# Optimization experiments

Hardware: AMD Instinct MI355X
Metric: run time of the kernel (lower is better)

## Reference

```python
import jax, jax.numpy as jnp
import numpy as np

N_USERS = 100000
N_ITEMS = 50000
NNZ = 1600000
DIM = 128


def setup_inputs() -> dict:
    key = jax.random.key(0)
    ks = jax.random.split(key, 6)
    user_emb = jax.random.normal(ks[0], (N_USERS, DIM), dtype=jnp.float32)
    item_emb = jax.random.normal(ks[1], (N_ITEMS, DIM), dtype=jnp.float32)
    hg_rows = jax.random.randint(ks[2], (NNZ,), 0, N_USERS, dtype=jnp.int32)
    hg_cols = jax.random.randint(ks[3], (NNZ,), 0, N_ITEMS, dtype=jnp.int32)
    hg_vals = jax.random.uniform(ks[4], (NNZ,), dtype=jnp.float32)
    # aggregation: nn.Linear(2*dim, dim) -> weight [dim, 2*dim], bias [dim]
    bound = 1.0 / np.sqrt(2 * DIM)
    W_agg = jax.random.uniform(ks[5], (DIM, 2 * DIM), minval=-bound, maxval=bound, dtype=jnp.float32)
    b_agg = jnp.zeros((DIM,), dtype=jnp.float32)
    return {"user_emb": user_emb, "item_emb": item_emb, "hg_rows": hg_rows,
            "hg_cols": hg_cols, "hg_vals": hg_vals, "W_agg": W_agg, "b_agg": b_agg}


def reference(user_emb, item_emb, hg_rows, hg_cols, hg_vals, W_agg, b_agg):
    n_users = user_emb.shape[0]
    n_items = item_emb.shape[0]
    # node_msg = H @ item_emb  (SpMM via gather + segment_sum)  [n_users, dim]
    gathered = hg_vals[:, None] * item_emb[hg_cols]          # [nnz, dim]
    node_msg = jax.ops.segment_sum(gathered, hg_rows, num_segments=n_users)
    # elementwise gate with user embedding
    edge_node_element = node_msg * user_emb                   # [n_users, dim]
    # msg = Linear(concat([node_msg, gated]))
    cat = jnp.concatenate([node_msg, edge_node_element], axis=1)  # [n_users, 2*dim]
    msg = cat @ W_agg.T + b_agg                               # [n_users, dim]
    # norm_emb = H.T @ msg  (transpose SpMM scatter-back)     [n_items, dim]
    scattered = hg_vals[:, None] * msg[hg_rows]               # [nnz, dim]
    norm_emb = jax.ops.segment_sum(scattered, hg_cols, num_segments=n_items)
    return (norm_emb, msg)
```

## Files before the change

kernel.cpp:

```cpp
#include <hip/hip_runtime.h>

#define DIM 128
#define NB 512

typedef short v8s __attribute__((ext_vector_type(8)));
typedef float v4f __attribute__((ext_vector_type(4)));

__device__ __forceinline__ unsigned short f2bf(float f) {
    unsigned int x = __float_as_uint(f);
    unsigned int r = ((x >> 16) & 1u) + 0x7fffu;
    return (unsigned short)((x + r) >> 16);
}
__device__ __forceinline__ float bf2f(short s) {
    return __uint_as_float(((unsigned)(unsigned short)s) << 16);
}


__global__ __launch_bounds__(256) void k_binA(const int* __restrict__ rows, const int* __restrict__ cols,
                                              int* __restrict__ Mu, int* __restrict__ Mi,
                                              int nnz, int chunk, int nbu, int nbi, int shu, int shi)
{
    __shared__ int hu[256], hi[256];
    int k = blockIdx.x, t = threadIdx.x;
    for (int j = t; j < nbu; j += 256) hu[j] = 0;
    for (int j = t; j < nbi; j += 256) hi[j] = 0;
    __syncthreads();
    int beg = k * chunk, end = min(beg + chunk, nnz);
    if (beg < end) {
        int beg4 = beg >> 2, end4 = end >> 2;
        for (int e4 = beg4 + t; e4 < end4; e4 += 256) {
            int4 r = reinterpret_cast<const int4*>(rows)[e4];
            int4 c = reinterpret_cast<const int4*>(cols)[e4];
            atomicAdd(&hu[r.x >> shu], 1); atomicAdd(&hu[r.y >> shu], 1);
            atomicAdd(&hu[r.z >> shu], 1); atomicAdd(&hu[r.w >> shu], 1);
            atomicAdd(&hi[c.x >> shi], 1); atomicAdd(&hi[c.y >> shi], 1);
            atomicAdd(&hi[c.z >> shi], 1); atomicAdd(&hi[c.w >> shi], 1);
        }
        for (int e = (end4 << 2) + t; e < end; e += 256) {
            atomicAdd(&hu[rows[e] >> shu], 1);
            atomicAdd(&hi[cols[e] >> shi], 1);
        }
    }
    __syncthreads();
    for (int j = t; j < nbu; j += 256) Mu[k * nbu + j] = hu[j];
    for (int j = t; j < nbi; j += 256) Mi[k * nbi + j] = hi[j];
}

__global__ __launch_bounds__(256) void k_binS1(int* __restrict__ M, int* __restrict__ tot,
                                               int nb, int nblk)
{
    __shared__ int ps[256];
    int j = blockIdx.x, t = threadIdx.x;
    int i0 = 2 * t, i1 = 2 * t + 1;
    int v0 = (i0 < nblk) ? M[i0 * nb + j] : 0;
    int v1 = (i1 < nblk) ? M[i1 * nb + j] : 0;
    ps[t] = v0 + v1;
    __syncthreads();
    for (int off = 1; off < 256; off <<= 1) {
        int x = (t >= off) ? ps[t - off] : 0;
        __syncthreads();
        ps[t] += x;
        __syncthreads();
    }
    int ep = ps[t] - (v0 + v1);
    if (i0 < nblk) M[i0 * nb + j] = ep;
    if (i1 < nblk) M[i1 * nb + j] = ep + v0;
    if (t == 255) tot[j] = ps[255];
}

__global__ __launch_bounds__(256) void k_binS2(const int* __restrict__ tot, int* __restrict__ base, int nb)
{
    __shared__ int s[256];
    int t = threadIdx.x;
    int v = (t < nb) ? tot[t] : 0;
    s[t] = v;
    __syncthreads();
    for (int off = 1; off < 256; off <<= 1) {
        int x = (t >= off) ? s[t - off] : 0;
        __syncthreads();
        s[t] += x;
        __syncthreads();
    }
    if (t < nb) base[t] = s[t] - v;
    if (t == 255) base[nb] = s[255];
}

__global__ __launch_bounds__(256) void k_binB(const int* __restrict__ rows, const int* __restrict__ cols,
                                              const float* __restrict__ vals,
                                              const int* __restrict__ Mu, const int* __restrict__ Mi,
                                              const int* __restrict__ base_u, const int* __restrict__ base_i,
                                              int2* __restrict__ bu, int2* __restrict__ bi,
                                              int nnz, int chunk, int nbu, int nbi, int shu, int shi)
{
    __shared__ int cu[256], ci[256];
    int k = blockIdx.x, t = threadIdx.x;
    for (int j = t; j < nbu; j += 256) cu[j] = Mu[k * nbu + j] + base_u[j];
    for (int j = t; j < nbi; j += 256) ci[j] = Mi[k * nbi + j] + base_i[j];
    __syncthreads();
    int mu = (1 << shu) - 1, mi = (1 << shi) - 1;
    int beg = k * chunk, end = min(beg + chunk, nnz);
    if (beg >= end) return;
    int beg4 = beg >> 2, end4 = end >> 2;
    for (int e4 = beg4 + t; e4 < end4; e4 += 256) {
        int4 r = reinterpret_cast<const int4*>(rows)[e4];
        int4 c = reinterpret_cast<const int4*>(cols)[e4];
        int4 v = reinterpret_cast<const int4*>(vals)[e4];
        int p;
        p = atomicAdd(&cu[r.x >> shu], 1); bu[p] = make_int2((c.x << shu) | (r.x & mu), v.x);
        p = atomicAdd(&ci[c.x >> shi], 1); bi[p] = make_int2((r.x << shi) | (c.x & mi), v.x);
        p = atomicAdd(&cu[r.y >> shu], 1); bu[p] = make_int2((c.y << shu) | (r.y & mu), v.y);
        p = atomicAdd(&ci[c.y >> shi], 1); bi[p] = make_int2((r.y << shi) | (c.y & mi), v.y);
        p = atomicAdd(&cu[r.z >> shu], 1); bu[p] = make_int2((c.z << shu) | (r.z & mu), v.z);
        p = atomicAdd(&ci[c.z >> shi], 1); bi[p] = make_int2((r.z << shi) | (c.z & mi), v.z);
        p = atomicAdd(&cu[r.w >> shu], 1); bu[p] = make_int2((c.w << shu) | (r.w & mu), v.w);
        p = atomicAdd(&ci[c.w >> shi], 1); bi[p] = make_int2((r.w << shi) | (c.w & mi), v.w);
    }
    for (int e = (end4 << 2) + t; e < end; e += 256) {
        int r = rows[e], c = cols[e];
        int v = reinterpret_cast<const int*>(vals)[e];
        int p;
        p = atomicAdd(&cu[r >> shu], 1); bu[p] = make_int2((c << shu) | (r & mu), v);
        p = atomicAdd(&ci[c >> shi], 1); bi[p] = make_int2((r << shi) | (c & mi), v);
    }
}

__global__ __launch_bounds__(256) void k_binC(const int2* __restrict__ binned,
                                              const int* __restrict__ base,
                                              int* __restrict__ ptr, int2* __restrict__ cs,
                                              int nrows, int sh, int total)
{
    __shared__ int hist[512];
    __shared__ int scn[512];
    __shared__ int psum[256];
    int j = blockIdx.x, t = threadIdx.x;
    int BR = 1 << sh;
    int row0 = j << sh;
    int beg = base[j], end = base[j + 1];
    for (int r = t; r < BR; r += 256) hist[r] = 0;
    __syncthreads();
    for (int e = beg + t; e < end; e += 256)
        atomicAdd(&hist[binned[e].x & (BR - 1)], 1);
    __syncthreads();
    int v0 = (2 * t < BR) ? hist[2 * t] : 0;
    int v1 = (2 * t + 1 < BR) ? hist[2 * t + 1] : 0;
    psum[t] = v0 + v1;
    __syncthreads();
    for (int off = 1; off < 256; off <<= 1) {
        int x = (t >= off) ? psum[t - off] : 0;
        __syncthreads();
        psum[t] += x;
        __syncthreads();
    }
    int ep = psum[t] - (v0 + v1);
    if (2 * t < BR) scn[2 * t] = ep;
    if (2 * t + 1 < BR) scn[2 * t + 1] = ep + v0;
    __syncthreads();
    for (int r = t; r < BR; r += 256) {
        int row = row0 + r;
        if (row < nrows) ptr[row] = beg + scn[r];
        hist[r] = 0;
    }
    if (j == 0 && t == 0) ptr[nrows] = total;
    __syncthreads();
    for (int e = beg + t; e < end; e += 256) {
        int2 rec = binned[e];
        int rl = rec.x & (BR - 1);
        int pos = beg + scn[rl] + atomicAdd(&hist[rl], 1);
        cs[pos] = make_int2(((unsigned)rec.x) >> sh, rec.y);
    }
}

__global__ void k_tobf(const float* __restrict__ in, unsigned short* __restrict__ out, int n8)
{
    int i = blockIdx.x * 256 + threadIdx.x;
    if (i >= n8) return;
    float4 a = reinterpret_cast<const float4*>(in)[2 * i];
    float4 c = reinterpret_cast<const float4*>(in)[2 * i + 1];
    uint4 o;
    o.x = (unsigned)f2bf(a.x) | ((unsigned)f2bf(a.y) << 16);
    o.y = (unsigned)f2bf(a.z) | ((unsigned)f2bf(a.w) << 16);
    o.z = (unsigned)f2bf(c.x) | ((unsigned)f2bf(c.y) << 16);
    o.w = (unsigned)f2bf(c.z) | ((unsigned)f2bf(c.w) << 16);
    reinterpret_cast<uint4*>(out)[i] = o;
}

__global__ __launch_bounds__(256) void k_spmm_bf(const int* __restrict__ ptr, const int2* __restrict__ pairs,
                                                 const unsigned short* __restrict__ src,
                                                 float* __restrict__ dst, int nrows)
{
    int r = blockIdx.x * 16 + (threadIdx.x >> 4);
    if (r >= nrows) return;
    int l = threadIdx.x & 15;
    int beg = ptr[r], end = ptr[r + 1];
    float a0[8], a1[8];
    #pragma unroll
    for (int k = 0; k < 8; ++k) { a0[k] = 0.f; a1[k] = 0.f; }
    int j = beg;
    for (; j + 1 < end; j += 2) {
        int2 p0 = pairs[j], p1 = pairs[j + 1];
        float v0 = __int_as_float(p0.y), v1 = __int_as_float(p1.y);
        v8s s0 = *reinterpret_cast<const v8s*>(src + (long long)p0.x * DIM + 8 * l);
        v8s s1 = *reinterpret_cast<const v8s*>(src + (long long)p1.x * DIM + 8 * l);
        #pragma unroll
        for (int k = 0; k < 8; ++k) {
            a0[k] += v0 * bf2f(s0[k]);
            a1[k] += v1 * bf2f(s1[k]);
        }
    }
    if (j < end) {
        int2 p0 = pairs[j];
        float v0 = __int_as_float(p0.y);
        v8s s0 = *reinterpret_cast<const v8s*>(src + (long long)p0.x * DIM + 8 * l);
        #pragma unroll
        for (int k = 0; k < 8; ++k) a0[k] += v0 * bf2f(s0[k]);
    }
    float4 o0, o1;
    o0.x = a0[0] + a1[0]; o0.y = a0[1] + a1[1]; o0.z = a0[2] + a1[2]; o0.w = a0[3] + a1[3];
    o1.x = a0[4] + a1[4]; o1.y = a0[5] + a1[5]; o1.z = a0[6] + a1[6]; o1.w = a0[7] + a1[7];
    float* dp = dst + (long long)r * DIM + 8 * l;
    *reinterpret_cast<float4*>(dp) = o0;
    *reinterpret_cast<float4*>(dp + 4) = o1;
}

__global__ __launch_bounds__(256) void k_spmm4(const int* __restrict__ ptr, const int2* __restrict__ pairs,
                                               const float* __restrict__ src, float* __restrict__ dst, int nrows)
{
    int r = blockIdx.x * 8 + (threadIdx.x >> 5);
    if (r >= nrows) return;
    int l = threadIdx.x & 31;
    int beg = ptr[r], end = ptr[r + 1];
    float4 a0 = {0.f, 0.f, 0.f, 0.f}, a1 = {0.f, 0.f, 0.f, 0.f};
    int j = beg;
    for (; j + 1 < end; j += 2) {
        int2 p0 = pairs[j], p1 = pairs[j + 1];
        float v0 = __int_as_float(p0.y), v1 = __int_as_float(p1.y);
        float4 s0 = *reinterpret_cast<const float4*>(src + (long long)p0.x * DIM + 4 * l);
        float4 s1 = *reinterpret_cast<const float4*>(src + (long long)p1.x * DIM + 4 * l);
        a0.x += v0 * s0.x; a0.y += v0 * s0.y; a0.z += v0 * s0.z; a0.w += v0 * s0.w;
        a1.x += v1 * s1.x; a1.y += v1 * s1.y; a1.z += v1 * s1.z; a1.w += v1 * s1.w;
    }
    if (j < end) {
        int2 p0 = pairs[j];
        float v0 = __int_as_float(p0.y);
        float4 s0 = *reinterpret_cast<const float4*>(src + (long long)p0.x * DIM + 4 * l);
        a0.x += v0 * s0.x; a0.y += v0 * s0.y; a0.z += v0 * s0.z; a0.w += v0 * s0.w;
    }
    a0.x += a1.x; a0.y += a1.y; a0.z += a1.z; a0.w += a1.w;
    *reinterpret_cast<float4*>(dst + (long long)r * DIM + 4 * l) = a0;
}

__global__ void k_bsw(const float* __restrict__ W, unsigned short* __restrict__ Bsw)
{
    int i = blockIdx.x * 256 + threadIdx.x;
    int kt = i >> 12;
    int rem = i & 4095;
    int c = rem >> 5;
    int kk = rem & 31;
    Bsw[i] = f2bf(W[c * 256 + kt * 32 + kk]);
}

__global__ __launch_bounds__(256) void k_msg5(const float* __restrict__ nm_in,
                                              const float* __restrict__ ue,
                                              const unsigned short* __restrict__ Bsw,
                                              const float* __restrict__ b,
                                              float* __restrict__ msg,
                                              unsigned short* __restrict__ msg_bf, int nu)
{
    __shared__ unsigned short cat[64 * 264];
    int tid = threadIdx.x;
    int u0 = blockIdx.x * 64;

    for (int idx = tid; idx < 2048; idx += 256) {
        int u = idx >> 5, d4 = idx & 31;
        float4 nm4 = make_float4(0.f, 0.f, 0.f, 0.f);
        float4 ue4 = make_float4(0.f, 0.f, 0.f, 0.f);
        if (u0 + u < nu) {
            long long p = (long long)(u0 + u) * DIM + d4 * 4;
            nm4 = *reinterpret_cast<const float4*>(nm_in + p);
            ue4 = *reinterpret_cast<const float4*>(ue + p);
        }
        unsigned short* row = cat + u * 264;
        uint2 nmp, gp;
        nmp.x = (unsigned)f2bf(nm4.x) | ((unsigned)f2bf(nm4.y) << 16);
        nmp.y = (unsigned)f2bf(nm4.z) | ((unsigned)f2bf(nm4.w) << 16);
        gp.x  = (unsigned)f2bf(nm4.x * ue4.x) | ((unsigned)f2bf(nm4.y * ue4.y) << 16);
        gp.y  = (unsigned)f2bf(nm4.z * ue4.z) | ((unsigned)f2bf(nm4.w * ue4.w) << 16);
        *reinterpret_cast<uint2*>(row + d4 * 4) = nmp;
        *reinterpret_cast<uint2*>(row + 128 + d4 * 4) = gp;
    }
    __syncthreads();

    int l = tid & 63, w = tid >> 6;
    int lr = l & 15, hi = l >> 4;
    v4f acc[8];
    #pragma unroll
    for (int ct = 0; ct < 8; ++ct) acc[ct] = (v4f){0.f, 0.f, 0.f, 0.f};

    const unsigned short* arow = cat + (w * 16 + lr) * 264;
    for (int kt = 0; kt < 8; ++kt) {
        v8s a = *reinterpret_cast<const v8s*>(arow + kt * 32 + hi * 8);
        #pragma unroll
        for (int ct = 0; ct < 8; ++ct) {
            v8s bb = *reinterpret_cast<const v8s*>(Bsw + kt * 4096 + (ct * 16 + lr) * 32 + hi * 8);
            acc[ct] = __builtin_amdgcn_mfma_f32_16x16x32_bf16(a, bb, acc[ct], 0, 0, 0);
        }
    }

    int ub = u0 + w * 16 + hi * 4;
    #pragma unroll
    for (int ct = 0; ct < 8; ++ct) {
        float bc = b[ct * 16 + lr];
        #pragma unroll
        for (int j = 0; j < 4; ++j) {
            int u = ub + j;
            if (u < nu) {
                float val = acc[ct][j] + bc;
                long long p = (long long)u * DIM + ct * 16 + lr;
                msg[p] = val;
                msg_bf[p] = f2bf(val);
            }
        }
    }
}

__global__ void k_wt(const float* __restrict__ W, float* __restrict__ Wt)
{
    int t = blockIdx.x * 256 + threadIdx.x;
    int k = t >> 7;
    int c = t & 127;
    Wt[t] = W[c * 256 + k];
}

#define UPB 32
#define CATP 260

__global__ __launch_bounds__(256) void k_msg4(const float* __restrict__ nm_in,
                                              const float* __restrict__ ue,
                                              const float* __restrict__ Wt,
                                              const float* __restrict__ b,
                                              float* __restrict__ msg, int nu)
{
    __shared__ float cat[UPB * CATP];
    int tid = threadIdx.x;
    int u0 = blockIdx.x * UPB;
    for (int idx = tid; idx < UPB * DIM; idx += 256) {
        int u = idx >> 7, d = idx & 127;
        float nm = 0.f, g = 0.f;
        if (u0 + u < nu) {
            long long p = (long long)(u0 + u) * DIM + d;
            nm = nm_in[p];
            g = nm * ue[p];
        }
        cat[u * CATP + d] = nm;
        cat[u * CATP + DIM + d] = g;
    }
    __syncthreads();

    int tc = tid & 31;
    int tu = tid >> 5;
    float acc[4][4];
    #pragma unroll
    for (int r = 0; r < 4; ++r)
        #pragma unroll
        for (int c = 0; c < 4; ++c) acc[r][c] = 0.f;

    const float* cbase = &cat[(tu * 4) * CATP];
    for (int k4 = 0; k4 < 64; ++k4) {
        float4 w[4];
        #pragma unroll
        for (int kk = 0; kk < 4; ++kk)
            w[kk] = *reinterpret_cast<const float4*>(Wt + (k4 * 4 + kk) * DIM + tc * 4);
        #pragma unroll
        for (int r = 0; r < 4; ++r) {
            float4 a = *reinterpret_cast<const float4*>(cbase + r * CATP + k4 * 4);
            acc[r][0] += a.x * w[0].x + a.y * w[1].x + a.z * w[2].x + a.w * w[3].x;
            acc[r][1] += a.x * w[0].y + a.y * w[1].y + a.z * w[2].y + a.w * w[3].y;
            acc[r][2] += a.x * w[0].z + a.y * w[1].z + a.z * w[2].z + a.w * w[3].z;
            acc[r][3] += a.x * w[0].w + a.y * w[1].w + a.z * w[2].w + a.w * w[3].w;
        }
    }

    float4 bb = *reinterpret_cast<const float4*>(b + tc * 4);
    #pragma unroll
    for (int r = 0; r < 4; ++r) {
        int u = u0 + tu * 4 + r;
        if (u < nu) {
            float4 o;
            o.x = acc[r][0] + bb.x; o.y = acc[r][1] + bb.y;
            o.z = acc[r][2] + bb.z; o.w = acc[r][3] + bb.w;
            *reinterpret_cast<float4*>(msg + (long long)u * DIM + tc * 4) = o;
        }
    }
}


__global__ void k_count(const int* __restrict__ rows, const int* __restrict__ cols,
                        int* __restrict__ cnt_u, int* __restrict__ cnt_i, int nnz4, int nnz)
{
    int i = blockIdx.x * blockDim.x + threadIdx.x;
    int stride = gridDim.x * blockDim.x;
    for (int e4 = i; e4 < nnz4; e4 += stride) {
        int4 r = reinterpret_cast<const int4*>(rows)[e4];
        int4 c = reinterpret_cast<const int4*>(cols)[e4];
        atomicAdd(&cnt_u[r.x], 1); atomicAdd(&cnt_u[r.y], 1);
        atomicAdd(&cnt_u[r.z], 1); atomicAdd(&cnt_u[r.w], 1);
        atomicAdd(&cnt_i[c.x], 1); atomicAdd(&cnt_i[c.y], 1);
        atomicAdd(&cnt_i[c.z], 1); atomicAdd(&cnt_i[c.w], 1);
    }
    for (int e = nnz4 * 4 + i; e < nnz; e += stride) {
        atomicAdd(&cnt_u[rows[e]], 1);
        atomicAdd(&cnt_i[cols[e]], 1);
    }
}

__global__ void k_scan1(const int* __restrict__ cnt, int* __restrict__ ptr,
                        int* __restrict__ partial, int n)
{
    __shared__ int s[256];
    int i = blockIdx.x * 256 + threadIdx.x;
    int v = (i < n) ? cnt[i] : 0;
    s[threadIdx.x] = v;
    __syncthreads();
    for (int off = 1; off < 256; off <<= 1) {
        int x = (threadIdx.x >= off) ? s[threadIdx.x - off] : 0;
        __syncthreads();
        s[threadIdx.x] += x;
        __syncthreads();
    }
    if (i < n) ptr[i] = s[threadIdx.x] - v;
    if (threadIdx.x == 255) partial[blockIdx.x] = s[255];
}

__global__ void k_scan2(int* __restrict__ partial, int n)
{
    __shared__ int s[512];
    int v = (threadIdx.x < (unsigned)n) ? partial[threadIdx.x] : 0;
    s[threadIdx.x] = v;
    __syncthreads();
    for (int off = 1; off < 512; off <<= 1) {
        int x = (threadIdx.x >= off) ? s[threadIdx.x - off] : 0;
        __syncthreads();
        s[threadIdx.x] += x;
        __syncthreads();
    }
    if (threadIdx.x < (unsigned)n) partial[threadIdx.x] = s[threadIdx.x] - v;
}

__global__ void k_scan3(int* __restrict__ ptr, const int* __restrict__ partial,
                        int* __restrict__ woff, int n, int total)
{
    int i = blockIdx.x * 256 + threadIdx.x;
    if (i < n) {
        int p = ptr[i] + partial[blockIdx.x];
        ptr[i] = p;
        woff[i] = p;
        if (i == n - 1) ptr[n] = total;
    }
}

__global__ void k_edge_scatter(const int* __restrict__ rows, const int* __restrict__ cols,
                               const float* __restrict__ vals,
                               int* __restrict__ woff_u, int* __restrict__ woff_i,
                               int2* __restrict__ cs_u, int2* __restrict__ cs_i,
                               int nnz4, int nnz)
{
    int i = blockIdx.x * blockDim.x + threadIdx.x;
    int stride = gridDim.x * blockDim.x;
    for (int e4 = i; e4 < nnz4; e4 += stride) {
        int4 r = reinterpret_cast<const int4*>(rows)[e4];
        int4 c = reinterpret_cast<const int4*>(cols)[e4];
        float4 v = reinterpret_cast<const float4*>(vals)[e4];
        int pu, pi;
        pu = atomicAdd(&woff_u[r.x], 1); cs_u[pu] = make_int2(c.x, __float_as_int(v.x));
        pi = atomicAdd(&woff_i[c.x], 1); cs_i[pi] = make_int2(r.x, __float_as_int(v.x));
        pu = atomicAdd(&woff_u[r.y], 1); cs_u[pu] = make_int2(c.y, __float_as_int(v.y));
        pi = atomicAdd(&woff_i[c.y], 1); cs_i[pi] = make_int2(r.y, __float_as_int(v.y));
        pu = atomicAdd(&woff_u[r.z], 1); cs_u[pu] = make_int2(c.z, __float_as_int(v.z));
        pi = atomicAdd(&woff_i[c.z], 1); cs_i[pi] = make_int2(r.z, __float_as_int(v.z));
        pu = atomicAdd(&woff_u[r.w], 1); cs_u[pu] = make_int2(c.w, __float_as_int(v.w));
        pi = atomicAdd(&woff_i[c.w], 1); cs_i[pi] = make_int2(r.w, __float_as_int(v.w));
    }
    for (int e = nnz4 * 4 + i; e < nnz; e += stride) {
        int r = rows[e], c = cols[e];
        float v = vals[e];
        int pu = atomicAdd(&woff_u[r], 1); cs_u[pu] = make_int2(c, __float_as_int(v));
        int pi = atomicAdd(&woff_i[c], 1); cs_i[pi] = make_int2(r, __float_as_int(v));
    }
}


__global__ void k_scatter(const int* __restrict__ didx, const int* __restrict__ sidx,
                          const float* __restrict__ vals, const float* __restrict__ src,
                          float* __restrict__ dst, long long nnz)
{
    long long t = (long long)blockIdx.x * blockDim.x + threadIdx.x;
    long long total = nnz * 32;
    if (t >= total) return;
    long long e = t >> 5;
    int d = (int)(t & 31) * 4;
    int si = sidx[e];
    int di = didx[e];
    float v = vals[e];
    const float4 s = *reinterpret_cast<const float4*>(src + (long long)si * DIM + d);
    float* p = dst + (long long)di * DIM + d;
    atomicAdd(p + 0, v * s.x);
    atomicAdd(p + 1, v * s.y);
    atomicAdd(p + 2, v * s.z);
    atomicAdd(p + 3, v * s.w);
}

__global__ void k_msg_simple(const float* __restrict__ user_emb, const float* __restrict__ W,
                             const float* __restrict__ b, float* __restrict__ msg)
{
    __shared__ float cat[2 * DIM];
    int u = blockIdx.x;
    int t = threadIdx.x;
    long long base = (long long)u * DIM;
    float nm = msg[base + t];
    float ue = user_emb[base + t];
    cat[t] = nm;
    cat[DIM + t] = nm * ue;
    __syncthreads();
    float acc = b[t];
    const float4* Wr = reinterpret_cast<const float4*>(W + (long long)t * 2 * DIM);
    const float4* c4 = reinterpret_cast<const float4*>(cat);
    #pragma unroll
    for (int k = 0; k < 2 * DIM / 4; ++k) {
        float4 w = Wr[k];
        float4 c = c4[k];
        acc += w.x * c.x + w.y * c.y + w.z * c.z + w.w * c.w;
    }
    msg[base + t] = acc;
}


extern "C" void kernel_launch(void* const* d_in, const int* in_sizes, int n_in,
                              void* d_out, int out_size, void* d_ws, size_t ws_size,
                              hipStream_t stream) {
    const float* user_emb = (const float*)d_in[0];
    const float* item_emb = (const float*)d_in[1];
    const int*   rows     = (const int*)d_in[2];
    const int*   cols     = (const int*)d_in[3];
    const float* vals     = (const float*)d_in[4];
    const float* W        = (const float*)d_in[5];
    const float* b        = (const float*)d_in[6];

    int nu = in_sizes[0] / DIM;
    int ni = in_sizes[1] / DIM;
    int nnz = in_sizes[2];

    float* norm_emb = (float*)d_out;
    float* msg      = (float*)d_out + (long long)ni * DIM;

    auto align256 = [](size_t x) { return (x + 255) & ~(size_t)255; };

    int shu = 0; while ((((long long)nu + (1LL << shu) - 1) >> shu) > 256) shu++;
    int shi = 0; while ((((long long)ni + (1LL << shi) - 1) >> shi) > 256) shi++;
    int nbu = (int)(((long long)nu + (1LL << shu) - 1) >> shu);
    int nbi = (int)(((long long)ni + (1LL << shi) - 1) >> shi);
    int chunk = (((nnz + NB - 1) / NB) + 3) & ~3;

    size_t off = 0;
    size_t o_bu    = off; off = align256(off + (size_t)nnz * 8);
    size_t o_bi    = off; off = align256(off + (size_t)nnz * 8);
    size_t o_csu   = off; off = align256(off + (size_t)nnz * 8);
    size_t o_Mu    = off; off = align256(off + (size_t)NB * nbu * 4);
    size_t o_Mi    = off; off = align256(off + (size_t)NB * nbi * 4);
    size_t o_totu  = off; off = align256(off + (size_t)nbu * 4);
    size_t o_toti  = off; off = align256(off + (size_t)nbi * 4);
    size_t o_baseu = off; off = align256(off + (size_t)(nbu + 1) * 4);
    size_t o_basei = off; off = align256(off + (size_t)(nbi + 1) * 4);
    size_t o_ptru  = off; off = align256(off + (size_t)(nu + 1) * 4);
    size_t o_ptri  = off; off = align256(off + (size_t)(ni + 1) * 4);
    size_t o_bsw   = off; off = align256(off + (size_t)32768 * 2);
    size_t need_binned = off;

    size_t itbf_need  = (size_t)ni * DIM * 2;
    size_t msgbf_need = (size_t)nu * DIM * 2;
    size_t o_itbf, o_msgbf;
    bool alias_it  = (o_csu - o_bi) >= itbf_need;
    bool alias_msg = (o_Mu - o_bi) >= msgbf_need;
    if (alias_it) o_itbf = o_bi;
    else { o_itbf = need_binned; need_binned = align256(need_binned + itbf_need); }
    if (alias_msg) o_msgbf = o_bi;
    else { o_msgbf = need_binned; need_binned = align256(need_binned + msgbf_need); }

    bool pack_ok = ((long long)ni < (1LL << (31 - shu))) && ((long long)nu < (1LL << (31 - shi)))
                   && (shu <= 9) && (shi <= 9);

    off = 0;
    size_t o_cs_u   = off; off = align256(off + (size_t)nnz * 8);
    size_t o_cs_i   = off; off = align256(off + (size_t)nnz * 8);
    size_t o_ptr_u  = off; off = align256(off + (size_t)(nu + 1) * 4);
    size_t o_ptr_i  = off; off = align256(off + (size_t)(ni + 1) * 4);
    size_t o_woff_u = off; off = align256(off + (size_t)nu * 4);
    size_t o_woff_i = off; off = align256(off + (size_t)ni * 4);
    size_t o_part_u = off; off = align256(off + 512 * 4);
    size_t o_part_i = off; off = align256(off + 512 * 4);
    size_t o_wt2    = off; off = align256(off + (size_t)256 * DIM * 4);
    size_t need_r5 = off;

    int npb_u = (nu + 255) / 256;
    int npb_i = (ni + 255) / 256;

    char* ws = (char*)d_ws;

    if (ws_size >= need_binned && pack_ok) {
        int2* bu     = (int2*)(ws + o_bu);
        int2* bi     = (int2*)(ws + o_bi);
        int2* cs_u   = (int2*)(ws + o_csu);
        int2* cs_i   = (int2*)(ws + o_bu);
        int*  Mu     = (int*)(ws + o_Mu);
        int*  Mi     = (int*)(ws + o_Mi);
        int*  totu   = (int*)(ws + o_totu);
        int*  toti   = (int*)(ws + o_toti);
        int*  baseu  = (int*)(ws + o_baseu);
        int*  basei  = (int*)(ws + o_basei);
        int*  ptr_u  = (int*)(ws + o_ptru);
        int*  ptr_i  = (int*)(ws + o_ptri);
        unsigned short* bsw   = (unsigned short*)(ws + o_bsw);
        unsigned short* itbf  = (unsigned short*)(ws + o_itbf);
        unsigned short* msgbf = (unsigned short*)(ws + o_msgbf);

        k_binA<<<NB, 256, 0, stream>>>(rows, cols, Mu, Mi, nnz, chunk, nbu, nbi, shu, shi);
        k_bsw<<<128, 256, 0, stream>>>(W, bsw);
        k_binS1<<<nbu, 256, 0, stream>>>(Mu, totu, nbu, NB);
        k_binS1<<<nbi, 256, 0, stream>>>(Mi, toti, nbi, NB);
        k_binS2<<<1, 256, 0, stream>>>(totu, baseu, nbu);
        k_binS2<<<1, 256, 0, stream>>>(toti, basei, nbi);
        k_binB<<<NB, 256, 0, stream>>>(rows, cols, vals, Mu, Mi, baseu, basei,
                                       bu, bi, nnz, chunk, nbu, nbi, shu, shi);
        k_binC<<<nbu, 256, 0, stream>>>(bu, baseu, ptr_u, cs_u, nu, shu, nnz);
        k_binC<<<nbi, 256, 0, stream>>>(bi, basei, ptr_i, cs_i, ni, shi, nnz);

        int n8i = ni * DIM / 8;
        k_tobf<<<(n8i + 255) / 256, 256, 0, stream>>>(item_emb, itbf, n8i);

        k_spmm_bf<<<(nu + 15) / 16, 256, 0, stream>>>(ptr_u, cs_u, itbf, msg, nu);
        k_msg5<<<(nu + 63) / 64, 256, 0, stream>>>(msg, user_emb, bsw, b, msg, msgbf, nu);
        k_spmm_bf<<<(ni + 15) / 16, 256, 0, stream>>>(ptr_i, cs_i, msgbf, norm_emb, ni);
    } else if (ws_size >= need_r5 && npb_u <= 512 && npb_i <= 512) {
        int2*  cs_u   = (int2*)(ws + o_cs_u);
        int2*  cs_i   = (int2*)(ws + o_cs_i);
        int*   ptr_u  = (int*)(ws + o_ptr_u);
        int*   ptr_i  = (int*)(ws + o_ptr_i);
        int*   woff_u = (int*)(ws + o_woff_u);
        int*   woff_i = (int*)(ws + o_woff_i);
        int*   part_u = (int*)(ws + o_part_u);
        int*   part_i = (int*)(ws + o_part_i);
        float* wt     = (float*)(ws + o_wt2);

        hipMemsetAsync(woff_u, 0, (size_t)nu * 4, stream);
        hipMemsetAsync(woff_i, 0, (size_t)ni * 4, stream);

        int nnz4 = nnz / 4;
        int gs = 1024;
        k_count<<<gs, 256, 0, stream>>>(rows, cols, woff_u, woff_i, nnz4, nnz);
        k_wt<<<(256 * DIM) / 256, 256, 0, stream>>>(W, wt);

        k_scan1<<<npb_u, 256, 0, stream>>>(woff_u, ptr_u, part_u, nu);
        k_scan1<<<npb_i, 256, 0, stream>>>(woff_i, ptr_i, part_i, ni);
        k_scan2<<<1, 512, 0, stream>>>(part_u, npb_u);
        k_scan2<<<1, 512, 0, stream>>>(part_i, npb_i);
        k_scan3<<<npb_u, 256, 0, stream>>>(ptr_u, part_u, woff_u, nu, nnz);
        k_scan3<<<npb_i, 256, 0, stream>>>(ptr_i, part_i, woff_i, ni, nnz);

        k_edge_scatter<<<gs, 256, 0, stream>>>(rows, cols, vals, woff_u, woff_i,
                                               cs_u, cs_i, nnz4, nnz);

        k_spmm4<<<(nu + 7) / 8, 256, 0, stream>>>(ptr_u, cs_u, item_emb, msg, nu);
        k_msg4<<<(nu + UPB - 1) / UPB, 256, 0, stream>>>(msg, user_emb, wt, b, msg, nu);
        k_spmm4<<<(ni + 7) / 8, 256, 0, stream>>>(ptr_i, cs_i, msg, norm_emb, ni);
    } else {
        hipMemsetAsync(d_out, 0, (size_t)out_size * sizeof(float), stream);
        long long tot = (long long)nnz * 32;
        int blk = 256;
        long long nblk = (tot + blk - 1) / blk;
        k_scatter<<<(int)nblk, blk, 0, stream>>>(rows, cols, vals, item_emb, msg, nnz);
        k_msg_simple<<<nu, DIM, 0, stream>>>(user_emb, W, b, msg);
        k_scatter<<<(int)nblk, blk, 0, stream>>>(cols, rows, vals, msg, norm_emb, nnz);
    }
}
```

Baseline: 278.6 us.

## Fuse user-side SpMM with gating and MFMA linear layer into one kernel

Adds a single-wavefront kernel that gathers bf16 item rows per user, applies the user-embedding gate, stages the concatenated bf16 row in shared memory and runs the 256x128 linear layer with MFMA, writing msg and its bf16 copy. This removes the fp32 node_msg write and re-read between the SpMM and linear kernels, plus one launch. The msg bf16 buffer gets its own workspace region so it no longer aliases the binning buffer still in use. The cost is 64-thread blocks, each thread walking four users serially, and a fallback to the old path when workspace is too small.

```diff
diff --git a/kernel.cpp b/kernel.cpp
--- a/kernel.cpp
+++ b/kernel.cpp
@@ -259,6 +259,101 @@
     Bsw[i] = f2bf(W[c * 256 + kt * 32 + kk]);
 }
 
+__global__ __launch_bounds__(64) void k_fused64(const int* __restrict__ ptr,
+                                                const int2* __restrict__ pairs,
+                                                const unsigned short* __restrict__ itbf,
+                                                const float* __restrict__ ue,
+                                                const unsigned short* __restrict__ Bsw,
+                                                const float* __restrict__ b,
+                                                float* __restrict__ msg,
+                                                unsigned short* __restrict__ msg_bf, int nu)
+{
+    __shared__ unsigned short cat[16 * 264];
+    int l = threadIdx.x;
+    int u0 = blockIdx.x * 16;
+    int lr = l & 15, hi = l >> 4;
+    int d = lr * 8;
+
+    #pragma unroll
+    for (int p = 0; p < 4; ++p) {
+        int ur = p * 4 + hi;
+        int u = u0 + ur;
+        float a0[8], a1[8];
+        #pragma unroll
+        for (int k = 0; k < 8; ++k) { a0[k] = 0.f; a1[k] = 0.f; }
+        float4 ue0 = make_float4(0.f,0.f,0.f,0.f), ue1 = make_float4(0.f,0.f,0.f,0.f);
+        if (u < nu) {
+            int beg = ptr[u], end = ptr[u + 1];
+            int j = beg;
+            for (; j + 1 < end; j += 2) {
+                int2 p0 = pairs[j], p1 = pairs[j + 1];
+                float v0 = __int_as_float(p0.y), v1 = __int_as_float(p1.y);
+                v8s s0 = *reinterpret_cast<const v8s*>(itbf + (long long)p0.x * DIM + d);
+                v8s s1 = *reinterpret_cast<const v8s*>(itbf + (long long)p1.x * DIM + d);
+                #pragma unroll
+                for (int k = 0; k < 8; ++k) {
+                    a0[k] += v0 * bf2f(s0[k]);
+                    a1[k] += v1 * bf2f(s1[k]);
+                }
+            }
+            if (j < end) {
+                int2 p0 = pairs[j];
+                float v0 = __int_as_float(p0.y);
+                v8s s0 = *reinterpret_cast<const v8s*>(itbf + (long long)p0.x * DIM + d);
+                #pragma unroll
+                for (int k = 0; k < 8; ++k) a0[k] += v0 * bf2f(s0[k]);
+            }
+            ue0 = *reinterpret_cast<const float4*>(ue + (long long)u * DIM + d);
+            ue1 = *reinterpret_cast<const float4*>(ue + (long long)u * DIM + d + 4);
+        }
+        float nm[8];
+        #pragma unroll
+        for (int k = 0; k < 8; ++k) nm[k] = a0[k] + a1[k];
+        float uev[8] = {ue0.x, ue0.y, ue0.z, ue0.w, ue1.x, ue1.y, ue1.z, ue1.w};
+        uint4 nmp, gp;
+        nmp.x = (unsigned)f2bf(nm[0]) | ((unsigned)f2bf(nm[1]) << 16);
+        nmp.y = (unsigned)f2bf(nm[2]) | ((unsigned)f2bf(nm[3]) << 16);
+        nmp.z = (unsigned)f2bf(nm[4]) | ((unsigned)f2bf(nm[5]) << 16);
+        nmp.w = (unsigned)f2bf(nm[6]) | ((unsigned)f2bf(nm[7]) << 16);
+        gp.x = (unsigned)f2bf(nm[0] * uev[0]) | ((unsigned)f2bf(nm[1] * uev[1]) << 16);
+        gp.y = (unsigned)f2bf(nm[2] * uev[2]) | ((unsigned)f2bf(nm[3] * uev[3]) << 16);
+        gp.z = (unsigned)f2bf(nm[4] * uev[4]) | ((unsigned)f2bf(nm[5] * uev[5]) << 16);
+        gp.w = (unsigned)f2bf(nm[6] * uev[6]) | ((unsigned)f2bf(nm[7] * uev[7]) << 16);
+        *reinterpret_cast<uint4*>(cat + ur * 264 + d) = nmp;
+        *reinterpret_cast<uint4*>(cat + ur * 264 + 128 + d) = gp;
+    }
+    __syncthreads();
+
+    v4f acc[8];
+    #pragma unroll
+    for (int ct = 0; ct < 8; ++ct) acc[ct] = (v4f){0.f, 0.f, 0.f, 0.f};
+    const unsigned short* arow = cat + lr * 264;
+    for (int kt = 0; kt < 8; ++kt) {
+        v8s a = *reinterpret_cast<const v8s*>(arow + kt * 32 + hi * 8);
+        #pragma unroll
+        for (int ct = 0; ct < 8; ++ct) {
+            v8s bb = *reinterpret_cast<const v8s*>(Bsw + kt * 4096 + (ct * 16 + lr) * 32 + hi * 8);
+            acc[ct] = __builtin_amdgcn_mfma_f32_16x16x32_bf16(a, bb, acc[ct], 0, 0, 0);
+        }
+    }
+
+    int ub = u0 + hi * 4;
+    #pragma unroll
+    for (int ct = 0; ct < 8; ++ct) {
+        float bc = b[ct * 16 + lr];
+        #pragma unroll
+        for (int j = 0; j < 4; ++j) {
+            int u = ub + j;
+            if (u < nu) {
+                float val = acc[ct][j] + bc;
+                long long p = (long long)u * DIM + ct * 16 + lr;
+                msg[p] = val;
+                msg_bf[p] = f2bf(val);
+            }
+        }
+    }
+}
+
 __global__ __launch_bounds__(256) void k_msg5(const float* __restrict__ nm_in,
                                               const float* __restrict__ ue,
                                               const unsigned short* __restrict__ Bsw,
@@ -573,17 +668,25 @@
     size_t o_ptru  = off; off = align256(off + (size_t)(nu + 1) * 4);
     size_t o_ptri  = off; off = align256(off + (size_t)(ni + 1) * 4);
     size_t o_bsw   = off; off = align256(off + (size_t)32768 * 2);
-    size_t need_binned = off;
+    size_t need_base = off;
 
     size_t itbf_need  = (size_t)ni * DIM * 2;
     size_t msgbf_need = (size_t)nu * DIM * 2;
-    size_t o_itbf, o_msgbf;
-    bool alias_it  = (o_csu - o_bi) >= itbf_need;
+    bool alias_it = (o_csu - o_bi) >= itbf_need;
+
+    size_t need_fused = need_base;
+    size_t o_msgbf_f = need_fused; need_fused = align256(need_fused + msgbf_need);
+    size_t o_itbf_f;
+    if (alias_it) o_itbf_f = o_bi;
+    else { o_itbf_f = need_fused; need_fused = align256(need_fused + itbf_need); }
+
+    size_t need_r9 = need_base;
     bool alias_msg = (o_Mu - o_bi) >= msgbf_need;
-    if (alias_it) o_itbf = o_bi;
-    else { o_itbf = need_binned; need_binned = align256(need_binned + itbf_need); }
-    if (alias_msg) o_msgbf = o_bi;
-    else { o_msgbf = need_binned; need_binned = align256(need_binned + msgbf_need); }
+    size_t o_itbf_9, o_msgbf_9;
+    if (alias_it) o_itbf_9 = o_bi;
+    else { o_itbf_9 = need_r9; need_r9 = align256(need_r9 + itbf_need); }
+    if (alias_msg) o_msgbf_9 = o_bi;
+    else { o_msgbf_9 = need_r9; need_r9 = align256(need_r9 + msgbf_need); }
 
     bool pack_ok = ((long long)ni < (1LL << (31 - shu))) && ((long long)nu < (1LL << (31 - shi)))
                    && (shu <= 9) && (shi <= 9);
@@ -605,7 +708,8 @@
 
     char* ws = (char*)d_ws;
 
-    if (ws_size >= need_binned && pack_ok) {
+    if (pack_ok && (ws_size >= need_fused || ws_size >= need_r9)) {
+        bool fused = (ws_size >= need_fused);
         int2* bu     = (int2*)(ws + o_bu);
         int2* bi     = (int2*)(ws + o_bi);
         int2* cs_u   = (int2*)(ws + o_csu);
@@ -619,8 +723,8 @@
         int*  ptr_u  = (int*)(ws + o_ptru);
         int*  ptr_i  = (int*)(ws + o_ptri);
         unsigned short* bsw   = (unsigned short*)(ws + o_bsw);
-        unsigned short* itbf  = (unsigned short*)(ws + o_itbf);
-        unsigned short* msgbf = (unsigned short*)(ws + o_msgbf);
+        unsigned short* itbf  = (unsigned short*)(ws + (fused ? o_itbf_f : o_itbf_9));
+        unsigned short* msgbf = (unsigned short*)(ws + (fused ? o_msgbf_f : o_msgbf_9));
 
         k_binA<<<NB, 256, 0, stream>>>(rows, cols, Mu, Mi, nnz, chunk, nbu, nbi, shu, shi);
         k_bsw<<<128, 256, 0, stream>>>(W, bsw);
@@ -636,8 +740,13 @@
         int n8i = ni * DIM / 8;
         k_tobf<<<(n8i + 255) / 256, 256, 0, stream>>>(item_emb, itbf, n8i);
 
-        k_spmm_bf<<<(nu + 15) / 16, 256, 0, stream>>>(ptr_u, cs_u, itbf, msg, nu);
-        k_msg5<<<(nu + 63) / 64, 256, 0, stream>>>(msg, user_emb, bsw, b, msg, msgbf, nu);
+        if (fused) {
+            k_fused64<<<(nu + 15) / 16, 64, 0, stream>>>(ptr_u, cs_u, itbf, user_emb,
+                                                         bsw, b, msg, msgbf, nu);
+        } else {
+            k_spmm_bf<<<(nu + 15) / 16, 256, 0, stream>>>(ptr_u, cs_u, itbf, msg, nu);
+            k_msg5<<<(nu + 63) / 64, 256, 0, stream>>>(msg, user_emb, bsw, b, msg, msgbf, nu);
+        }
         k_spmm_bf<<<(ni + 15) / 16, 256, 0, stream>>>(ptr_i, cs_i, msgbf, norm_emb, ni);
     } else if (ws_size >= need_r5 && npb_u <= 512 && npb_i <= 512) {
         int2*  cs_u   = (int2*)(ws + o_cs_u);
```

Result: no change. 275.4 us (-1.2%).

## Fuse user SpMM gather into MFMA linear kernel and merge binning launches

Applied to the files above, without the earlier changes.

Fuses the user-side SpMM gather with the gate and the bf16 MFMA linear layer, so node_msg no longer makes an fp32 round trip through global memory. The binning scan and compaction kernels for users and items are merged into single launches to cut launch count. The SpMM gather is rewritten so each 16-lane group handles two rows, with pair indices loaded cooperatively and broadcast by shuffles, giving 16 outstanding loads per iteration. The workspace now gives cs_i and msgbf their own regions instead of aliasing, which raises the memory footprint.

```diff
diff --git a/kernel.cpp b/kernel.cpp
--- a/kernel.cpp
+++ b/kernel.cpp
@@ -46,14 +46,18 @@
     for (int j = t; j < nbi; j += 256) Mi[k * nbi + j] = hi[j];
 }
 
-__global__ __launch_bounds__(256) void k_binS1(int* __restrict__ M, int* __restrict__ tot,
-                                               int nb, int nblk)
+__global__ __launch_bounds__(256) void k_binS1m(int* __restrict__ Mu, int* __restrict__ totu, int nbu,
+                                                int* __restrict__ Mi, int* __restrict__ toti, int nbi,
+                                                int nblk)
 {
     __shared__ int ps[256];
     int j = blockIdx.x, t = threadIdx.x;
+    int* M; int* tot; int nb; int col;
+    if (j < nbu) { M = Mu; tot = totu; nb = nbu; col = j; }
+    else         { M = Mi; tot = toti; nb = nbi; col = j - nbu; }
     int i0 = 2 * t, i1 = 2 * t + 1;
-    int v0 = (i0 < nblk) ? M[i0 * nb + j] : 0;
-    int v1 = (i1 < nblk) ? M[i1 * nb + j] : 0;
+    int v0 = (i0 < nblk) ? M[i0 * nb + col] : 0;
+    int v1 = (i1 < nblk) ? M[i1 * nb + col] : 0;
     ps[t] = v0 + v1;
     __syncthreads();
     for (int off = 1; off < 256; off <<= 1) {
@@ -63,15 +67,19 @@
         __syncthreads();
     }
     int ep = ps[t] - (v0 + v1);
-    if (i0 < nblk) M[i0 * nb + j] = ep;
-    if (i1 < nblk) M[i1 * nb + j] = ep + v0;
-    if (t == 255) tot[j] = ps[255];
-}
-
-__global__ __launch_bounds__(256) void k_binS2(const int* __restrict__ tot, int* __restrict__ base, int nb)
+    if (i0 < nblk) M[i0 * nb + col] = ep;
+    if (i1 < nblk) M[i1 * nb + col] = ep + v0;
+    if (t == 255) tot[col] = ps[255];
+}
+
+__global__ __launch_bounds__(256) void k_binS2m(const int* __restrict__ totu, int* __restrict__ baseu, int nbu,
+                                                const int* __restrict__ toti, int* __restrict__ basei, int nbi)
 {
     __shared__ int s[256];
     int t = threadIdx.x;
+    const int* tot; int* base; int nb;
+    if (blockIdx.x == 0) { tot = totu; base = baseu; nb = nbu; }
+    else                 { tot = toti; base = basei; nb = nbi; }
     int v = (t < nb) ? tot[t] : 0;
     s[t] = v;
     __syncthreads();
@@ -124,18 +132,22 @@
     }
 }
 
-__global__ __launch_bounds__(256) void k_binC(const int2* __restrict__ binned,
-                                              const int* __restrict__ base,
-                                              int* __restrict__ ptr, int2* __restrict__ cs,
-                                              int nrows, int sh, int total)
+__global__ __launch_bounds__(256) void k_binCm(const int2* __restrict__ bu, const int* __restrict__ baseu,
+                                               int* __restrict__ ptru, int2* __restrict__ csu, int nu_, int shu,
+                                               const int2* __restrict__ bi, const int* __restrict__ basei,
+                                               int* __restrict__ ptri, int2* __restrict__ csi, int ni_, int shi,
+                                               int nbu, int total)
 {
     __shared__ int hist[512];
     __shared__ int scn[512];
     __shared__ int psum[256];
     int j = blockIdx.x, t = threadIdx.x;
+    const int2* binned; const int* base; int* ptr; int2* cs; int nrows, sh, lj;
+    if (j < nbu) { binned = bu; base = baseu; ptr = ptru; cs = csu; nrows = nu_; sh = shu; lj = j; }
+    else         { binned = bi; base = basei; ptr = ptri; cs = csi; nrows = ni_; sh = shi; lj = j - nbu; }
     int BR = 1 << sh;
-    int row0 = j << sh;
-    int beg = base[j], end = base[j + 1];
+    int row0 = lj << sh;
+    int beg = base[lj], end = base[lj + 1];
     for (int r = t; r < BR; r += 256) hist[r] = 0;
     __syncthreads();
     for (int e = beg + t; e < end; e += 256)
@@ -160,7 +172,7 @@
         if (row < nrows) ptr[row] = beg + scn[r];
         hist[r] = 0;
     }
-    if (j == 0 && t == 0) ptr[nrows] = total;
+    if (lj == 0 && t == 0) ptr[nrows] = total;
     __syncthreads();
     for (int e = beg + t; e < end; e += 256) {
         int2 rec = binned[e];
@@ -184,42 +196,81 @@
     reinterpret_cast<uint4*>(out)[i] = o;
 }
 
+__device__ __forceinline__ void gather8x2(const int2* __restrict__ pairs,
+                                          const unsigned short* __restrict__ src,
+                                          int b0, int e0, int b1, int e1,
+                                          int lr, int gb,
+                                          float* __restrict__ acc0,
+                                          float* __restrict__ acc1)
+{
+    while (b0 < e0 || b1 < e1) {
+        int2 pl = make_int2(0, 0);
+        if (lr < 8) {
+            if (b0 + lr < e0) pl = pairs[b0 + lr];
+        } else {
+            int o = lr - 8;
+            if (b1 + o < e1) pl = pairs[b1 + o];
+        }
+        int   idx[16];
+        float vv[16];
+        #pragma unroll
+        for (int e = 0; e < 16; ++e) {
+            idx[e] = __shfl(pl.x, gb + e, 64);
+            vv[e]  = __int_as_float(__shfl(pl.y, gb + e, 64));
+        }
+        v8s sa[8], sb[8];
+        #pragma unroll
+        for (int e = 0; e < 8; ++e)
+            sa[e] = *reinterpret_cast<const v8s*>(src + (long long)idx[e] * DIM + 8 * lr);
+        #pragma unroll
+        for (int e = 0; e < 8; ++e)
+            sb[e] = *reinterpret_cast<const v8s*>(src + (long long)idx[8 + e] * DIM + 8 * lr);
+        #pragma unroll
+        for (int e = 0; e < 8; ++e) {
+            #pragma unroll
+            for (int k = 0; k < 8; ++k)
+                acc0[k] += vv[e] * bf2f(sa[e][k]);
+        }
+        #pragma unroll
+        for (int e = 0; e < 8; ++e) {
+            #pragma unroll
+            for (int k = 0; k < 8; ++k)
+                acc1[k] += vv[8 + e] * bf2f(sb[e][k]);
+        }
+        b0 += 8; b1 += 8;
+    }
+}
+
 __global__ __launch_bounds__(256) void k_spmm_bf(const int* __restrict__ ptr, const int2* __restrict__ pairs,
                                                  const unsigned short* __restrict__ src,
                                                  float* __restrict__ dst, int nrows)
 {
-    int r = blockIdx.x * 16 + (threadIdx.x >> 4);
-    if (r >= nrows) return;
-    int l = threadIdx.x & 15;
-    int beg = ptr[r], end = ptr[r + 1];
-    float a0[8], a1[8];
+    int g = threadIdx.x >> 4;
+    int r0 = blockIdx.x * 32 + g;
+    int r1 = r0 + 16;
+    int lr = threadIdx.x & 15;
+    int gb = (threadIdx.x & 63) & ~15;
+    int b0 = 0, e0 = 0, b1 = 0, e1 = 0;
+    if (r0 < nrows) { b0 = ptr[r0]; e0 = ptr[r0 + 1]; }
+    if (r1 < nrows) { b1 = ptr[r1]; e1 = ptr[r1 + 1]; }
+    float acc0[8], acc1[8];
     #pragma unroll
-    for (int k = 0; k < 8; ++k) { a0[k] = 0.f; a1[k] = 0.f; }
-    int j = beg;
-    for (; j + 1 < end; j += 2) {
-        int2 p0 = pairs[j], p1 = pairs[j + 1];
-        float v0 = __int_as_float(p0.y), v1 = __int_as_float(p1.y);
-        v8s s0 = *reinterpret_cast<const v8s*>(src + (long long)p0.x * DIM + 8 * l);
-        v8s s1 = *reinterpret_cast<const v8s*>(src + (long long)p1.x * DIM + 8 * l);
-        #pragma unroll
-        for (int k = 0; k < 8; ++k) {
-            a0[k] += v0 * bf2f(s0[k]);
-            a1[k] += v1 * bf2f(s1[k]);
-        }
-    }
-    if (j < end) {
-        int2 p0 = pairs[j];
-        float v0 = __int_as_float(p0.y);
-        v8s s0 = *reinterpret_cast<const v8s*>(src + (long long)p0.x * DIM + 8 * l);
-        #pragma unroll
-        for (int k = 0; k < 8; ++k) a0[k] += v0 * bf2f(s0[k]);
-    }
-    float4 o0, o1;
-    o0.x = a0[0] + a1[0]; o0.y = a0[1] + a1[1]; o0.z = a0[2] + a1[2]; o0.w = a0[3] + a1[3];
-    o1.x = a0[4] + a1[4]; o1.y = a0[5] + a1[5]; o1.z = a0[6] + a1[6]; o1.w = a0[7] + a1[7];
-    float* dp = dst + (long long)r * DIM + 8 * l;
-    *reinterpret_cast<float4*>(dp) = o0;
-    *reinterpret_cast<float4*>(dp + 4) = o1;
+    for (int k = 0; k < 8; ++k) { acc0[k] = 0.f; acc1[k] = 0.f; }
+    gather8x2(pairs, src, b0, e0, b1, e1, lr, gb, acc0, acc1);
+    if (r0 < nrows) {
+        float* dp = dst + (long long)r0 * DIM + 8 * lr;
+        float4 o0 = {acc0[0], acc0[1], acc0[2], acc0[3]};
+        float4 o1 = {acc0[4], acc0[5], acc0[6], acc0[7]};
+        *reinterpret_cast<float4*>(dp) = o0;
+        *reinterpret_cast<float4*>(dp + 4) = o1;
+    }
+    if (r1 < nrows) {
+        float* dp = dst + (long long)r1 * DIM + 8 * lr;
+        float4 o0 = {acc1[0], acc1[1], acc1[2], acc1[3]};
+        float4 o1 = {acc1[4], acc1[5], acc1[6], acc1[7]};
+        *reinterpret_cast<float4*>(dp) = o0;
+        *reinterpret_cast<float4*>(dp + 4) = o1;
+    }
 }
 
 __global__ __launch_bounds__(256) void k_spmm4(const int* __restrict__ ptr, const int2* __restrict__ pairs,
@@ -259,62 +310,99 @@
     Bsw[i] = f2bf(W[c * 256 + kt * 32 + kk]);
 }
 
-__global__ __launch_bounds__(256) void k_msg5(const float* __restrict__ nm_in,
-                                              const float* __restrict__ ue,
-                                              const unsigned short* __restrict__ Bsw,
-                                              const float* __restrict__ b,
-                                              float* __restrict__ msg,
-                                              unsigned short* __restrict__ msg_bf, int nu)
-{
-    __shared__ unsigned short cat[64 * 264];
+__global__ __launch_bounds__(256) void k_fused(const int* __restrict__ ptr,
+                                               const int2* __restrict__ pairs,
+                                               const unsigned short* __restrict__ itbf,
+                                               const float* __restrict__ ue,
+                                               const unsigned short* __restrict__ Bsw,
+                                               const float* __restrict__ b,
+                                               float* __restrict__ msg,
+                                               unsigned short* __restrict__ msg_bf, int nu)
+{
+    __shared__ unsigned short cat[4][16 * 264];
     int tid = threadIdx.x;
-    int u0 = blockIdx.x * 64;
-
-    for (int idx = tid; idx < 2048; idx += 256) {
-        int u = idx >> 5, d4 = idx & 31;
-        float4 nm4 = make_float4(0.f, 0.f, 0.f, 0.f);
-        float4 ue4 = make_float4(0.f, 0.f, 0.f, 0.f);
-        if (u0 + u < nu) {
-            long long p = (long long)(u0 + u) * DIM + d4 * 4;
-            nm4 = *reinterpret_cast<const float4*>(nm_in + p);
-            ue4 = *reinterpret_cast<const float4*>(ue + p);
-        }
-        unsigned short* row = cat + u * 264;
-        uint2 nmp, gp;
-        nmp.x = (unsigned)f2bf(nm4.x) | ((unsigned)f2bf(nm4.y) << 16);
-        nmp.y = (unsigned)f2bf(nm4.z) | ((unsigned)f2bf(nm4.w) << 16);
-        gp.x  = (unsigned)f2bf(nm4.x * ue4.x) | ((unsigned)f2bf(nm4.y * ue4.y) << 16);
-        gp.y  = (unsigned)f2bf(nm4.z * ue4.z) | ((unsigned)f2bf(nm4.w * ue4.w) << 16);
-        *reinterpret_cast<uint2*>(row + d4 * 4) = nmp;
-        *reinterpret_cast<uint2*>(row + 128 + d4 * 4) = gp;
-    }
-    __syncthreads();
-
-    int l = tid & 63, w = tid >> 6;
+    int w = tid >> 6, l = tid & 63;
     int lr = l & 15, hi = l >> 4;
-    v4f acc[8];
+    int gb = l & ~15;
+    int d = lr * 8;
+    int uw = blockIdx.x * 64 + w * 16;
+    unsigned short* mycat = &cat[w][0];
+
     #pragma unroll
-    for (int ct = 0; ct < 8; ++ct) acc[ct] = (v4f){0.f, 0.f, 0.f, 0.f};
-
-    const unsigned short* arow = cat + (w * 16 + lr) * 264;
+    for (int pp = 0; pp < 2; ++pp) {
+        int ur0 = pp * 4 + hi;
+        int ur1 = ur0 + 8;
+        int ua = uw + ur0, ub = uw + ur1;
+        float acc0[8], acc1[8];
+        #pragma unroll
+        for (int k = 0; k < 8; ++k) { acc0[k] = 0.f; acc1[k] = 0.f; }
+        float uev0[8], uev1[8];
+        #pragma unroll
+        for (int k = 0; k < 8; ++k) { uev0[k] = 0.f; uev1[k] = 0.f; }
+        int b0 = 0, e0 = 0, b1 = 0, e1 = 0;
+        if (ua < nu) {
+            float4 x0 = *reinterpret_cast<const float4*>(ue + (long long)ua * DIM + d);
+            float4 x1 = *reinterpret_cast<const float4*>(ue + (long long)ua * DIM + d + 4);
+            uev0[0] = x0.x; uev0[1] = x0.y; uev0[2] = x0.z; uev0[3] = x0.w;
+            uev0[4] = x1.x; uev0[5] = x1.y; uev0[6] = x1.z; uev0[7] = x1.w;
+            b0 = ptr[ua]; e0 = ptr[ua + 1];
+        }
+        if (ub < nu) {
+            float4 x0 = *reinterpret_cast<const float4*>(ue + (long long)ub * DIM + d);
+            float4 x1 = *reinterpret_cast<const float4*>(ue + (long long)ub * DIM + d + 4);
+            uev1[0] = x0.x; uev1[1] = x0.y; uev1[2] = x0.z; uev1[3] = x0.w;
+            uev1[4] = x1.x; uev1[5] = x1.y; uev1[6] = x1.z; uev1[7] = x1.w;
+            b1 = ptr[ub]; e1 = ptr[ub + 1];
+        }
+        gather8x2(pairs, itbf, b0, e0, b1, e1, lr, gb, acc0, acc1);
+
+        uint4 nmp, gp;
+        nmp.x = (unsigned)f2bf(acc0[0]) | ((unsigned)f2bf(acc0[1]) << 16);
+        nmp.y = (unsigned)f2bf(acc0[2]) | ((unsigned)f2bf(acc0[3]) << 16);
+        nmp.z = (unsigned)f2bf(acc0[4]) | ((unsigned)f2bf(acc0[5]) << 16);
+        nmp.w = (unsigned)f2bf(acc0[6]) | ((unsigned)f2bf(acc0[7]) << 16);
+        gp.x = (unsigned)f2bf(acc0[0] * uev0[0]) | ((unsigned)f2bf(acc0[1] * uev0[1]) << 16);
+        gp.y = (unsigned)f2bf(acc0[2] * uev0[2]) | ((unsigned)f2bf(acc0[3] * uev0[3]) << 16);
+        gp.z = (unsigned)f2bf(acc0[4] * uev0[4]) | ((unsigned)f2bf(acc0[5] * uev0[5]) << 16);
+        gp.w = (unsigned)f2bf(acc0[6] * uev0[6]) | ((unsigned)f2bf(acc0[7] * uev0[7]) << 16);
+        *reinterpret_cast<uint4*>(mycat + ur0 * 264 + d) = nmp;
+        *reinterpret_cast<uint4*>(mycat + ur0 * 264 + 128 + d) = gp;
+
+        nmp.x = (unsigned)f2bf(acc1[0]) | ((unsigned)f2bf(acc1[1]) << 16);
+        nmp.y = (unsigned)f2bf(acc1[2]) | ((unsigned)f2bf(acc1[3]) << 16);
+        nmp.z = (unsigned)f2bf(acc1[4]) | ((unsigned)f2bf(acc1[5]) << 16);
+        nmp.w = (unsigned)f2bf(acc1[6]) | ((unsigned)f2bf(acc1[7]) << 16);
+        gp.x = (unsigned)f2bf(acc1[0] * uev1[0]) | ((unsigned)f2bf(acc1[1] * uev1[1]) << 16);
+        gp.y = (unsigned)f2bf(acc1[2] * uev1[2]) | ((unsigned)f2bf(acc1[3] * uev1[3]) << 16);
+        gp.z = (unsigned)f2bf(acc1[4] * uev1[4]) | ((unsigned)f2bf(acc1[5] * uev1[5]) << 16);
+        gp.w = (unsigned)f2bf(acc1[6] * uev1[6]) | ((unsigned)f2bf(acc1[7] * uev1[7]) << 16);
+        *reinterpret_cast<uint4*>(mycat + ur1 * 264 + d) = nmp;
+        *reinterpret_cast<uint4*>(mycat + ur1 * 264 + 128 + d) = gp;
+    }
+    __syncthreads();
+
+    v4f facc[8];
+    #pragma unroll
+    for (int ct = 0; ct < 8; ++ct) facc[ct] = (v4f){0.f, 0.f, 0.f, 0.f};
+    const unsigned short* arow = mycat + lr * 264;
     for (int kt = 0; kt < 8; ++kt) {
         v8s a = *reinterpret_cast<const v8s*>(arow + kt * 32 + hi * 8);
         #pragma unroll
         for (int ct = 0; ct < 8; ++ct) {
             v8s bb = *reinterpret_cast<const v8s*>(Bsw + kt * 4096 + (ct * 16 + lr) * 32 + hi * 8);
-            acc[ct] = __builtin_amdgcn_mfma_f32_16x16x32_bf16(a, bb, acc[ct], 0, 0, 0);
-        }
-    }
-
-    int ub = u0 + w * 16 + hi * 4;
+            facc[ct] = __builtin_amdgcn_mfma_f32_16x16x32_bf16(a, bb, facc[ct], 0, 0, 0);
+        }
+    }
+
+    int ubase = uw + hi * 4;
     #pragma unroll
     for (int ct = 0; ct < 8; ++ct) {
         float bc = b[ct * 16 + lr];
         #pragma unroll
         for (int j = 0; j < 4; ++j) {
-            int u = ub + j;
+            int u = ubase + j;
             if (u < nu) {
-                float val = acc[ct][j] + bc;
+                float val = facc[ct][j] + bc;
                 long long p = (long long)u * DIM + ct * 16 + lr;
                 msg[p] = val;
                 msg_bf[p] = f2bf(val);
@@ -564,6 +652,7 @@
     size_t o_bu    = off; off = align256(off + (size_t)nnz * 8);
     size_t o_bi    = off; off = align256(off + (size_t)nnz * 8);
     size_t o_csu   = off; off = align256(off + (size_t)nnz * 8);
+    size_t o_csi   = off; off = align256(off + (size_t)nnz * 8);
     size_t o_Mu    = off; off = align256(off + (size_t)NB * nbu * 4);
     size_t o_Mi    = off; off = align256(off + (size_t)NB * nbi * 4);
     size_t o_totu  = off; off = align256(off + (size_t)nbu * 4);
@@ -573,17 +662,14 @@
     size_t o_ptru  = off; off = align256(off + (size_t)(nu + 1) * 4);
     size_t o_ptri  = off; off = align256(off + (size_t)(ni + 1) * 4);
     size_t o_bsw   = off; off = align256(off + (size_t)32768 * 2);
-    size_t need_binned = off;
-
-    size_t itbf_need  = (size_t)ni * DIM * 2;
-    size_t msgbf_need = (size_t)nu * DIM * 2;
-    size_t o_itbf, o_msgbf;
-    bool alias_it  = (o_csu - o_bi) >= itbf_need;
-    bool alias_msg = (o_Mu - o_bi) >= msgbf_need;
+    size_t o_msgbf = off; off = align256(off + (size_t)nu * DIM * 2);
+    size_t need_fused = off;
+
+    size_t itbf_need = (size_t)ni * DIM * 2;
+    bool alias_it = ((o_csu - o_bi) >= itbf_need);
+    size_t o_itbf;
     if (alias_it) o_itbf = o_bi;
-    else { o_itbf = need_binned; need_binned = align256(need_binned + itbf_need); }
-    if (alias_msg) o_msgbf = o_bi;
-    else { o_msgbf = need_binned; need_binned = align256(need_binned + msgbf_need); }
+    else { o_itbf = need_fused; need_fused = align256(need_fused + itbf_need); }
 
     bool pack_ok = ((long long)ni < (1LL << (31 - shu))) && ((long long)nu < (1LL << (31 - shi)))
                    && (shu <= 9) && (shi <= 9);
@@ -605,11 +691,11 @@
 
     char* ws = (char*)d_ws;
 
-    if (ws_size >= need_binned && pack_ok) {
+    if (pack_ok && ws_size >= need_fused) {
         int2* bu     = (int2*)(ws + o_bu);
         int2* bi     = (int2*)(ws + o_bi);
         int2* cs_u   = (int2*)(ws + o_csu);
-        int2* cs_i   = (int2*)(ws + o_bu);
+        int2* cs_i   = (int2*)(ws + o_csi);
         int*  Mu     = (int*)(ws + o_Mu);
         int*  Mi     = (int*)(ws + o_Mi);
         int*  totu   = (int*)(ws + o_totu);
@@ -619,26 +705,25 @@
         int*  ptr_u  = (int*)(ws + o_ptru);
         int*  ptr_i  = (int*)(ws + o_ptri);
         unsigned short* bsw   = (unsigned short*)(ws + o_bsw);
+        unsigned short* msgbf = (unsigned short*)(ws + o_msgbf);
         unsigned short* itbf  = (unsigned short*)(ws + o_itbf);
-        unsigned short* msgbf = (unsigned short*)(ws + o_msgbf);
 
         k_binA<<<NB, 256, 0, stream>>>(rows, cols, Mu, Mi, nnz, chunk, nbu, nbi, shu, shi);
         k_bsw<<<128, 256, 0, stream>>>(W, bsw);
-        k_binS1<<<nbu, 256, 0, stream>>>(Mu, totu, nbu, NB);
-        k_binS1<<<nbi, 256, 0, stream>>>(Mi, toti, nbi, NB);
-        k_binS2<<<1, 256, 0, stream>>>(totu, baseu, nbu);
-        k_binS2<<<1, 256, 0, stream>>>(toti, basei, nbi);
+        k_binS1m<<<nbu + nbi, 256, 0, stream>>>(Mu, totu, nbu, Mi, toti, nbi, NB);
+        k_binS2m<<<2, 256, 0, stream>>>(totu, baseu, nbu, toti, basei, nbi);
         k_binB<<<NB, 256, 0, stream>>>(rows, cols, vals, Mu, Mi, baseu, basei,
                                        bu, bi, nnz, chunk, nbu, nbi, shu, shi);
-        k_binC<<<nbu, 256, 0, stream>>>(bu, baseu, ptr_u, cs_u, nu, shu, nnz);
-        k_binC<<<nbi, 256, 0, stream>>>(bi, basei, ptr_i, cs_i, ni, shi, nnz);
+        k_binCm<<<nbu + nbi, 256, 0, stream>>>(bu, baseu, ptr_u, cs_u, nu, shu,
+                                               bi, basei, ptr_i, cs_i, ni, shi,
+                                               nbu, nnz);
 
         int n8i = ni * DIM / 8;
         k_tobf<<<(n8i + 255) / 256, 256, 0, stream>>>(item_emb, itbf, n8i);
 
-        k_spmm_bf<<<(nu + 15) / 16, 256, 0, stream>>>(ptr_u, cs_u, itbf, msg, nu);
-        k_msg5<<<(nu + 63) / 64, 256, 0, stream>>>(msg, user_emb, bsw, b, msg, msgbf, nu);
-        k_spmm_bf<<<(ni + 15) / 16, 256, 0, stream>>>(ptr_i, cs_i, msgbf, norm_emb, ni);
+        k_fused<<<(nu + 63) / 64, 256, 0, stream>>>(ptr_u, cs_u, itbf, user_emb,
+                                                    bsw, b, msg, msgbf, nu);
+        k_spmm_bf<<<(ni + 31) / 32, 256, 0, stream>>>(ptr_i, cs_i, msgbf, norm_emb, ni);
     } else if (ws_size >= need_r5 && npb_u <= 512 && npb_i <= 512) {
         int2*  cs_u   = (int2*)(ws + o_cs_u);
         int2*  cs_i   = (int2*)(ws + o_cs_i);
```

After: 255.6 us. 1.09x faster.
